# Performance work log

Measured on AMD Instinct MI355X. Metric: run time of the kernel, lower is better.

The kernel has to match this reference:

```python
import jax, jax.numpy as jnp
import numpy as np

B, T, D, H = 4096, 512, 1, 64

def _uniform(k, shape, scale):
    return jax.random.uniform(k, shape, jnp.float32, -scale, scale)

def setup_inputs() -> dict:
    key = jax.random.key(0)
    ks = jax.random.split(key, 12)
    s = 1.0 / np.sqrt(H)  # torch nn.LSTM init scale
    return {
        "x": jax.random.normal(ks[0], (B, T, D), jnp.float32),
        # layer 0 (input_size=D)
        "W_ih0": _uniform(ks[1], (4 * H, D), s),
        "W_hh0": _uniform(ks[2], (4 * H, H), s),
        "b_ih0": _uniform(ks[3], (4 * H,), s),
        "b_hh0": _uniform(ks[4], (4 * H,), s),
        # layer 1 (input_size=H)
        "W_ih1": _uniform(ks[5], (4 * H, H), s),
        "W_hh1": _uniform(ks[6], (4 * H, H), s),
        "b_ih1": _uniform(ks[7], (4 * H,), s),
        "b_hh1": _uniform(ks[8], (4 * H,), s),
        # final projection to scalar
        "W_fc": _uniform(ks[9], (1, H), s),
        "b_fc": _uniform(ks[10], (1,), s),
    }

def _lstm_layer(x_seq, W_ih, W_hh, b_ih, b_hh):
    # x_seq: (B, T, Din) -> hidden sequence (B, T, H). Gate order: i, f, g, o.
    b, t, _ = x_seq.shape
    h = W_hh.shape[1]
    # precompute input contribution for all timesteps: (T, B, 4H)
    x_proj = jnp.einsum('btd,gd->tbg', x_seq, W_ih) + b_ih + b_hh
    Whh_T = W_hh.T  # (H, 4H)

    def step(carry, xp):
        h_t, c_t = carry
        gates = xp + h_t @ Whh_T  # (B, 4H)
        i_g, f_g, g_g, o_g = jnp.split(gates, 4, axis=-1)
        i_g = jax.nn.sigmoid(i_g)
        f_g = jax.nn.sigmoid(f_g)
        g_g = jnp.tanh(g_g)
        o_g = jax.nn.sigmoid(o_g)
        c_t = f_g * c_t + i_g * g_g
        h_t = o_g * jnp.tanh(c_t)
        return (h_t, c_t), h_t

    h0 = jnp.zeros((b, h), x_seq.dtype)
    (_, _), hs = jax.lax.scan(step, (h0, h0), x_proj)  # hs: (T, B, H)
    return jnp.swapaxes(hs, 0, 1)

def reference(x, W_ih0, W_hh0, b_ih0, b_hh0, W_ih1, W_hh1, b_ih1, b_hh1, W_fc, b_fc):
    h1 = _lstm_layer(x, W_ih0, W_hh0, b_ih0, b_hh0)   # (B, T, H)
    h2 = _lstm_layer(h1, W_ih1, W_hh1, b_ih1, b_hh1)  # (B, T, H)
    last = h2[:, -1, :]                                # (B, H)
    return last @ W_fc.T + b_fc                        # (B, 1)
```

## Files before the change

### kernel.cpp

```cpp
#include <hip/hip_runtime.h>


#define TT 512
#define HH 64
#define NB 16
#define XP 516

typedef __bf16 bf16_t;
typedef bf16_t bf16x8 __attribute__((ext_vector_type(8)));
typedef float  f32x4  __attribute__((ext_vector_type(4)));
typedef float  f32x2  __attribute__((ext_vector_type(2)));

#define MFMA(A, B, C) __builtin_amdgcn_mfma_f32_16x16x32_bf16((A), (B), (C), 0, 0, 0)
#define RCPF(x) __builtin_amdgcn_rcpf(x)

#if __has_builtin(__builtin_amdgcn_exp2f)
#define EXP2F(x) __builtin_amdgcn_exp2f(x)
#else
__device__ __forceinline__ float EXP2F(float x) {
    float r;
    asm volatile("v_exp_f32 %0, %1" : "=v"(r) : "v"(x));
    return r;
}
#endif

#define SC_IFO (-1.4426950408889634f)
#define SC_G   ( 2.8853900817779268f)

__device__ __forceinline__ unsigned short f32_to_bf16_rne(float f) {
    unsigned int u = __builtin_bit_cast(unsigned int, f);
    unsigned int r = u + 0x7fffu + ((u >> 16) & 1u);
    return (unsigned short)(r >> 16);
}
__device__ __forceinline__ bf16_t bits_to_bf16(unsigned short u) {
    return __builtin_bit_cast(bf16_t, u);
}
__device__ __forceinline__ void build_frag_scaled(const float* __restrict__ p, float sc,
                                                  bf16x8& w) {
    const float4 a = *(const float4*)p;
    const float4 b = *(const float4*)(p + 4);
    float v[8] = {a.x, a.y, a.z, a.w, b.x, b.y, b.z, b.w};
#pragma unroll
    for (int jj = 0; jj < 8; ++jj)
        w[jj] = bits_to_bf16(f32_to_bf16_rne(v[jj] * sc));
}

__device__ __forceinline__ f32x2 exp2v(f32x2 v) {
    f32x2 r; r[0] = EXP2F(v[0]); r[1] = EXP2F(v[1]); return r;
}
__device__ __forceinline__ f32x2 rcpv(f32x2 v) {
    f32x2 r; r[0] = RCPF(v[0]); r[1] = RCPF(v[1]); return r;
}
__device__ __forceinline__ f32x2 cell2(const f32x4 a0, const f32x4 a1, f32x2* c) {
    f32x2 is = {a0[0], a1[0]}, fs = {a0[1], a1[1]};
    f32x2 gs = {a0[2], a1[2]}, os = {a0[3], a1[3]};
    const f32x2 pf = exp2v(fs);
    const f32x2 fg = rcpv(1.0f + pf);
    const f32x2 pi = exp2v(is);
    const f32x2 e2 = exp2v(gs);
    const f32x2 z  = (e2 - 1.0f) * rcpv((1.0f + pi) * (1.0f + e2));
    *c = fg * (*c) + z;
    const f32x2 po  = exp2v(os);
    const f32x2 e2c = exp2v((*c) * SC_G);
    return (e2c - 1.0f) * rcpv((1.0f + po) * (1.0f + e2c));
}

__device__ __forceinline__ int imin2(int a, int b) { return a < b ? a : b; }
__device__ __forceinline__ int min4of(const int* f) {
    const int4 v = *(const int4*)f;
    return imin2(imin2(v.x, v.y), imin2(v.z, v.w));
}
__device__ __forceinline__ int min8of(const int* f) {
    const int4 a = *(const int4*)f;
    const int4 b = *(const int4*)(f + 4);
    return imin2(imin2(imin2(a.x, a.y), imin2(a.z, a.w)),
                 imin2(imin2(b.x, b.y), imin2(b.z, b.w)));
}

#define SPIN_FUSED(F0, F1, C0, C1)                                              \
    do {                                                                        \
        __builtin_amdgcn_s_setprio(0);                                          \
        for (;;) {                                                              \
            asm volatile("" ::: "memory");                                      \
            if ((min4of(F0) >= (C0)) & (min8of(F1) >= (C1))) break;             \
            asm volatile("" ::: "memory");                                      \
            if ((min4of(F0) >= (C0)) & (min8of(F1) >= (C1))) break;             \
            __builtin_amdgcn_s_sleep(1);                                        \
        }                                                                       \
        __builtin_amdgcn_s_setprio(1);                                          \
    } while (0)

__global__ __launch_bounds__(768, 3)
void lstm_1t_kernel(const float* __restrict__ x,
                    const float* __restrict__ Wih0, const float* __restrict__ Whh0,
                    const float* __restrict__ bih0, const float* __restrict__ bhh0,
                    const float* __restrict__ Wih1, const float* __restrict__ Whh1,
                    const float* __restrict__ bih1, const float* __restrict__ bhh1,
                    const float* __restrict__ Wfc,  const float* __restrict__ bfc,
                    float* __restrict__ out)
{
    __shared__ float xbuf[NB][XP];
    __shared__ unsigned short h0r[8][NB][64];
    __shared__ unsigned short h1r[2][NB][64];
    __shared__ float h1fin[HH][NB + 1];
    __shared__ __align__(16) int f0[4];
    __shared__ __align__(16) int f1[8];

    const int tid  = threadIdx.x;
    const int wv   = tid >> 6;
    const int lane = tid & 63;
    const int m    = lane & 15;
    const int q    = lane >> 4;
    const int m7   = m & 7;
    const int b0   = blockIdx.x * NB;
    const bool isL0 = (wv < 4);

    for (int i = tid; i < NB * TT / 4; i += 768) {
        const int b  = i >> 7;
        const int t4 = i & 127;
        *(float4*)&xbuf[b][t4 * 4] = *(const float4*)&x[(size_t)(b0 + b) * TT + t4 * 4];
    }
    for (int i = tid; i < 8 * NB * 64; i += 768) (&h0r[0][0][0])[i] = 0;
    for (int i = tid; i < 2 * NB * 64; i += 768) (&h1r[0][0][0])[i] = 0;
    if (tid < 4) f0[tid] = -1;
    else if (tid < 12) f1[tid - 4] = -1;

    int roff[2];
#pragma unroll
    for (int kt = 0; kt < 2; ++kt)
        roff[kt] = m * 64 + (((4 * kt + q) ^ m7) * 8);

    const int gate_m = m & 3;
    const float scA  = (gate_m == 2) ? SC_G : SC_IFO;
    unsigned short* const H0 = &h0r[0][0][0];
    unsigned short* const H1 = &h1r[0][0][0];

    __syncthreads();

    __builtin_amdgcn_s_setprio(1);

    if (isL0) {
        const int w = wv;
        bf16x8 Ah[4][2];
        f32x4 bb0s[4], wx0s[4];
        int woff[4];
#pragma unroll
        for (int tau = 0; tau < 4; ++tau) {
            const int rowA = 64 * gate_m + 16 * w + 4 * tau + (m >> 2);
#pragma unroll
            for (int kt = 0; kt < 2; ++kt)
                build_frag_scaled(&Whh0[rowA * HH + kt * 32 + q * 8], scA, Ah[tau][kt]);
#pragma unroll
            for (int r = 0; r < 4; ++r) {
                const int row = 64 * r + 16 * w + 4 * tau + q;
                const float sc = (r == 2) ? SC_G : SC_IFO;
                bb0s[tau][r] = (bih0[row] + bhh0[row]) * sc;
                wx0s[tau][r] = Wih0[row] * sc;
            }
            const int u = 16 * w + 4 * tau + q;
            woff[tau] = m * 64 + (((u >> 3) ^ m7) * 8) + (u & 7);
        }

        f32x2 cA = {0.f, 0.f}, cB = {0.f, 0.f};

#pragma unroll 1
        for (int t = 0; t < TT; ++t) {
            asm volatile("" ::: "memory");
            const int c0 = t - 1;
            const int c1 = t - 8;
            const int rdy = (min4of(f0) >= c0) & (min8of(f1) >= c1);

            const float xv = xbuf[m][t];
            f32x4 a[4];
#pragma unroll
            for (int tau = 0; tau < 4; ++tau) {
#pragma unroll
                for (int r = 0; r < 4; ++r)
                    a[tau][r] = __builtin_fmaf(xv, wx0s[tau][r], bb0s[tau][r]);
            }

            if (!rdy) SPIN_FUSED(f0, f1, c0, c1);
            asm volatile("" ::: "memory");

            const int rs = ((t - 1) & 7) * (NB * 64);
            bf16x8 h0[2];
            h0[0] = *(const bf16x8*)(H0 + rs + roff[0]);
            h0[1] = *(const bf16x8*)(H0 + rs + roff[1]);

#pragma unroll
            for (int tau = 0; tau < 4; ++tau) {
                f32x4 z = {0.f, 0.f, 0.f, 0.f};
                a[tau] = MFMA(Ah[tau][0], h0[0], a[tau]);
                z      = MFMA(Ah[tau][1], h0[1], z);
                a[tau] = a[tau] + z;
            }

            const f32x2 hv0 = cell2(a[0], a[1], &cA);
            const f32x2 hv1 = cell2(a[2], a[3], &cB);

            const int ws = (t & 7) * (NB * 64);
            H0[ws + woff[0]] = f32_to_bf16_rne(hv0[0]);
            H0[ws + woff[1]] = f32_to_bf16_rne(hv0[1]);
            H0[ws + woff[2]] = f32_to_bf16_rne(hv1[0]);
            H0[ws + woff[3]] = f32_to_bf16_rne(hv1[1]);

            asm volatile("s_waitcnt lgkmcnt(0)" ::: "memory");
            if (lane == 0) *(volatile int*)&f0[w] = t;
        }
    } else {
        const int uW = wv - 4;
        bf16x8 Ah[2][4];
        f32x4 bb1s[2];
        int woff[2], uu[2];
#pragma unroll
        for (int tau = 0; tau < 2; ++tau) {
            const int rowA = 64 * gate_m + 8 * uW + 4 * tau + (m >> 2);
#pragma unroll
            for (int kt = 0; kt < 2; ++kt)
                build_frag_scaled(&Wih1[rowA * HH + kt * 32 + q * 8], scA, Ah[tau][kt]);
#pragma unroll
            for (int kt = 0; kt < 2; ++kt)
                build_frag_scaled(&Whh1[rowA * HH + kt * 32 + q * 8], scA, Ah[tau][2 + kt]);
#pragma unroll
            for (int r = 0; r < 4; ++r) {
                const int row = 64 * r + 8 * uW + 4 * tau + q;
                const float sc = (r == 2) ? SC_G : SC_IFO;
                bb1s[tau][r] = (bih1[row] + bhh1[row]) * sc;
            }
            const int u = 8 * uW + 4 * tau + q;
            uu[tau]   = u;
            woff[tau] = m * 64 + (((u >> 3) ^ m7) * 8) + (u & 7);
        }

        f32x2 c1v = {0.f, 0.f};

#pragma unroll 1
        for (int t = 0; t < TT; ++t) {
            asm volatile("" ::: "memory");
            const int c0 = t;
            const int c1 = t - 1;
            if (!((min4of(f0) >= c0) & (min8of(f1) >= c1)))
                SPIN_FUSED(f0, f1, c0, c1);
            asm volatile("" ::: "memory");

            const int rs0 = (t & 7) * (NB * 64);
            const int rs1 = ((t - 1) & 1) * (NB * 64);
            bf16x8 h0[2], h1[2];
            h0[0] = *(const bf16x8*)(H0 + rs0 + roff[0]);
            h0[1] = *(const bf16x8*)(H0 + rs0 + roff[1]);
            h1[0] = *(const bf16x8*)(H1 + rs1 + roff[0]);
            h1[1] = *(const bf16x8*)(H1 + rs1 + roff[1]);

            f32x4 a[2];
#pragma unroll
            for (int tau = 0; tau < 2; ++tau) {
                f32x4 p = bb1s[tau];
                f32x4 s = {0.f, 0.f, 0.f, 0.f};
                p = MFMA(Ah[tau][0], h0[0], p);
                p = MFMA(Ah[tau][1], h0[1], p);
                s = MFMA(Ah[tau][2], h1[0], s);
                s = MFMA(Ah[tau][3], h1[1], s);
                a[tau] = p + s;
            }

            const f32x2 hv = cell2(a[0], a[1], &c1v);
            if (t == TT - 1) {
                h1fin[uu[0]][m] = hv[0];
                h1fin[uu[1]][m] = hv[1];
            }
            const int ws = (t & 1) * (NB * 64);
            H1[ws + woff[0]] = f32_to_bf16_rne(hv[0]);
            H1[ws + woff[1]] = f32_to_bf16_rne(hv[1]);

            asm volatile("s_waitcnt lgkmcnt(0)" ::: "memory");
            if (lane == 0) *(volatile int*)&f1[uW] = t;
        }
    }

    __syncthreads();

    if (tid < NB) {
        float sacc = bfc[0];
#pragma unroll
        for (int u = 0; u < HH; ++u) sacc = fmaf(h1fin[u][tid], Wfc[u], sacc);
        out[b0 + tid] = sacc;
    }
}

extern "C" void kernel_launch(void* const* d_in, const int* in_sizes, int n_in,
                              void* d_out, int out_size, void* d_ws, size_t ws_size,
                              hipStream_t stream) {
    const float* x    = (const float*)d_in[0];
    const float* Wih0 = (const float*)d_in[1];
    const float* Whh0 = (const float*)d_in[2];
    const float* bih0 = (const float*)d_in[3];
    const float* bhh0 = (const float*)d_in[4];
    const float* Wih1 = (const float*)d_in[5];
    const float* Whh1 = (const float*)d_in[6];
    const float* bih1 = (const float*)d_in[7];
    const float* bhh1 = (const float*)d_in[8];
    const float* Wfc  = (const float*)d_in[9];
    const float* bfc  = (const float*)d_in[10];

    lstm_1t_kernel<<<dim3(4096 / NB), dim3(768), 0, stream>>>(
        x, Wih0, Whh0, bih0, bhh0, Wih1, Whh1, bih1, bhh1, Wfc, bfc, (float*)d_out);
}
```

Measured before the change: 492.4 us.

## Split layer-0 across eight waves and split layer-1 waits per input

Raises the block to 1024 threads so layer 0 runs on eight waves with two hidden tiles each instead of four waves with four tiles, shortening each wave's per-step critical path. Layer-1 waves now wait only on the layer-0 flags, issue the input-projection MFMAs, and only then wait on their own recurrent flags before the recurrent MFMAs. This overlaps some of the layer-1 dependency wait with useful work. In exchange there are more waves per block, more flag polling, and possibly fewer resident blocks per CU given the register budget.

```diff
diff --git a/kernel.cpp b/kernel.cpp
--- a/kernel.cpp
+++ b/kernel.cpp
@@ -66,10 +66,6 @@
 }
 
 __device__ __forceinline__ int imin2(int a, int b) { return a < b ? a : b; }
-__device__ __forceinline__ int min4of(const int* f) {
-    const int4 v = *(const int4*)f;
-    return imin2(imin2(v.x, v.y), imin2(v.z, v.w));
-}
 __device__ __forceinline__ int min8of(const int* f) {
     const int4 a = *(const int4*)f;
     const int4 b = *(const int4*)(f + 4);
@@ -77,20 +73,33 @@
                  imin2(imin2(b.x, b.y), imin2(b.z, b.w)));
 }
 
-#define SPIN_FUSED(F0, F1, C0, C1)                                              \
+#define SPIN_BOTH(F0, F1, C0, C1)                                               \
     do {                                                                        \
         __builtin_amdgcn_s_setprio(0);                                          \
         for (;;) {                                                              \
             asm volatile("" ::: "memory");                                      \
-            if ((min4of(F0) >= (C0)) & (min8of(F1) >= (C1))) break;             \
+            if ((min8of(F0) >= (C0)) & (min8of(F1) >= (C1))) break;             \
             asm volatile("" ::: "memory");                                      \
-            if ((min4of(F0) >= (C0)) & (min8of(F1) >= (C1))) break;             \
+            if ((min8of(F0) >= (C0)) & (min8of(F1) >= (C1))) break;             \
             __builtin_amdgcn_s_sleep(1);                                        \
         }                                                                       \
         __builtin_amdgcn_s_setprio(1);                                          \
     } while (0)
 
-__global__ __launch_bounds__(768, 3)
+#define SPIN_ONE(F, C)                                                          \
+    do {                                                                        \
+        __builtin_amdgcn_s_setprio(0);                                          \
+        for (;;) {                                                              \
+            asm volatile("" ::: "memory");                                      \
+            if (min8of(F) >= (C)) break;                                        \
+            asm volatile("" ::: "memory");                                      \
+            if (min8of(F) >= (C)) break;                                        \
+            __builtin_amdgcn_s_sleep(1);                                        \
+        }                                                                       \
+        __builtin_amdgcn_s_setprio(1);                                          \
+    } while (0)
+
+__global__ __launch_bounds__(1024, 4)
 void lstm_1t_kernel(const float* __restrict__ x,
                     const float* __restrict__ Wih0, const float* __restrict__ Whh0,
                     const float* __restrict__ bih0, const float* __restrict__ bhh0,
@@ -103,7 +112,7 @@
     __shared__ unsigned short h0r[8][NB][64];
     __shared__ unsigned short h1r[2][NB][64];
     __shared__ float h1fin[HH][NB + 1];
-    __shared__ __align__(16) int f0[4];
+    __shared__ __align__(16) int f0[8];
     __shared__ __align__(16) int f1[8];
 
     const int tid  = threadIdx.x;
@@ -113,17 +122,17 @@
     const int q    = lane >> 4;
     const int m7   = m & 7;
     const int b0   = blockIdx.x * NB;
-    const bool isL0 = (wv < 4);
-
-    for (int i = tid; i < NB * TT / 4; i += 768) {
+    const bool isL0 = (wv < 8);
+
+    for (int i = tid; i < NB * TT / 4; i += 1024) {
         const int b  = i >> 7;
         const int t4 = i & 127;
         *(float4*)&xbuf[b][t4 * 4] = *(const float4*)&x[(size_t)(b0 + b) * TT + t4 * 4];
     }
-    for (int i = tid; i < 8 * NB * 64; i += 768) (&h0r[0][0][0])[i] = 0;
-    for (int i = tid; i < 2 * NB * 64; i += 768) (&h1r[0][0][0])[i] = 0;
-    if (tid < 4) f0[tid] = -1;
-    else if (tid < 12) f1[tid - 4] = -1;
+    for (int i = tid; i < 8 * NB * 64; i += 1024) (&h0r[0][0][0])[i] = 0;
+    for (int i = tid; i < 2 * NB * 64; i += 1024) (&h1r[0][0][0])[i] = 0;
+    if (tid < 8) f0[tid] = -1;
+    else if (tid < 16) f1[tid - 8] = -1;
 
     int roff[2];
 #pragma unroll
@@ -141,45 +150,45 @@
 
     if (isL0) {
         const int w = wv;
-        bf16x8 Ah[4][2];
-        f32x4 bb0s[4], wx0s[4];
-        int woff[4];
-#pragma unroll
-        for (int tau = 0; tau < 4; ++tau) {
-            const int rowA = 64 * gate_m + 16 * w + 4 * tau + (m >> 2);
+        bf16x8 Ah[2][2];
+        f32x4 bb0s[2], wx0s[2];
+        int woff[2];
+#pragma unroll
+        for (int tau = 0; tau < 2; ++tau) {
+            const int rowA = 64 * gate_m + 8 * w + 4 * tau + (m >> 2);
 #pragma unroll
             for (int kt = 0; kt < 2; ++kt)
                 build_frag_scaled(&Whh0[rowA * HH + kt * 32 + q * 8], scA, Ah[tau][kt]);
 #pragma unroll
             for (int r = 0; r < 4; ++r) {
-                const int row = 64 * r + 16 * w + 4 * tau + q;
+                const int row = 64 * r + 8 * w + 4 * tau + q;
                 const float sc = (r == 2) ? SC_G : SC_IFO;
                 bb0s[tau][r] = (bih0[row] + bhh0[row]) * sc;
                 wx0s[tau][r] = Wih0[row] * sc;
             }
-            const int u = 16 * w + 4 * tau + q;
+            const int u = 8 * w + 4 * tau + q;
             woff[tau] = m * 64 + (((u >> 3) ^ m7) * 8) + (u & 7);
         }
 
-        f32x2 cA = {0.f, 0.f}, cB = {0.f, 0.f};
+        f32x2 cA = {0.f, 0.f};
 
 #pragma unroll 1
         for (int t = 0; t < TT; ++t) {
             asm volatile("" ::: "memory");
             const int c0 = t - 1;
             const int c1 = t - 8;
-            const int rdy = (min4of(f0) >= c0) & (min8of(f1) >= c1);
+            const int rdy = (min8of(f0) >= c0) & (min8of(f1) >= c1);
 
             const float xv = xbuf[m][t];
-            f32x4 a[4];
-#pragma unroll
-            for (int tau = 0; tau < 4; ++tau) {
+            f32x4 a[2];
+#pragma unroll
+            for (int tau = 0; tau < 2; ++tau) {
 #pragma unroll
                 for (int r = 0; r < 4; ++r)
                     a[tau][r] = __builtin_fmaf(xv, wx0s[tau][r], bb0s[tau][r]);
             }
 
-            if (!rdy) SPIN_FUSED(f0, f1, c0, c1);
+            if (!rdy) SPIN_BOTH(f0, f1, c0, c1);
             asm volatile("" ::: "memory");
 
             const int rs = ((t - 1) & 7) * (NB * 64);
@@ -188,27 +197,24 @@
             h0[1] = *(const bf16x8*)(H0 + rs + roff[1]);
 
 #pragma unroll
-            for (int tau = 0; tau < 4; ++tau) {
+            for (int tau = 0; tau < 2; ++tau) {
                 f32x4 z = {0.f, 0.f, 0.f, 0.f};
                 a[tau] = MFMA(Ah[tau][0], h0[0], a[tau]);
                 z      = MFMA(Ah[tau][1], h0[1], z);
                 a[tau] = a[tau] + z;
             }
 
-            const f32x2 hv0 = cell2(a[0], a[1], &cA);
-            const f32x2 hv1 = cell2(a[2], a[3], &cB);
+            const f32x2 hv = cell2(a[0], a[1], &cA);
 
             const int ws = (t & 7) * (NB * 64);
-            H0[ws + woff[0]] = f32_to_bf16_rne(hv0[0]);
-            H0[ws + woff[1]] = f32_to_bf16_rne(hv0[1]);
-            H0[ws + woff[2]] = f32_to_bf16_rne(hv1[0]);
-            H0[ws + woff[3]] = f32_to_bf16_rne(hv1[1]);
+            H0[ws + woff[0]] = f32_to_bf16_rne(hv[0]);
+            H0[ws + woff[1]] = f32_to_bf16_rne(hv[1]);
 
             asm volatile("s_waitcnt lgkmcnt(0)" ::: "memory");
             if (lane == 0) *(volatile int*)&f0[w] = t;
         }
     } else {
-        const int uW = wv - 4;
+        const int uW = wv - 8;
         bf16x8 Ah[2][4];
         f32x4 bb1s[2];
         int woff[2], uu[2];
@@ -237,30 +243,33 @@
 #pragma unroll 1
         for (int t = 0; t < TT; ++t) {
             asm volatile("" ::: "memory");
-            const int c0 = t;
-            const int c1 = t - 1;
-            if (!((min4of(f0) >= c0) & (min8of(f1) >= c1)))
-                SPIN_FUSED(f0, f1, c0, c1);
+            if (min8of(f0) < t) SPIN_ONE(f0, t);
             asm volatile("" ::: "memory");
 
             const int rs0 = (t & 7) * (NB * 64);
-            const int rs1 = ((t - 1) & 1) * (NB * 64);
-            bf16x8 h0[2], h1[2];
+            bf16x8 h0[2];
             h0[0] = *(const bf16x8*)(H0 + rs0 + roff[0]);
             h0[1] = *(const bf16x8*)(H0 + rs0 + roff[1]);
+
+            f32x4 a[2];
+#pragma unroll
+            for (int tau = 0; tau < 2; ++tau) {
+                a[tau] = MFMA(Ah[tau][0], h0[0], bb1s[tau]);
+                a[tau] = MFMA(Ah[tau][1], h0[1], a[tau]);
+            }
+
+            if (min8of(f1) < t - 1) SPIN_ONE(f1, t - 1);
+            asm volatile("" ::: "memory");
+
+            const int rs1 = ((t - 1) & 1) * (NB * 64);
+            bf16x8 h1[2];
             h1[0] = *(const bf16x8*)(H1 + rs1 + roff[0]);
             h1[1] = *(const bf16x8*)(H1 + rs1 + roff[1]);
 
-            f32x4 a[2];
 #pragma unroll
             for (int tau = 0; tau < 2; ++tau) {
-                f32x4 p = bb1s[tau];
-                f32x4 s = {0.f, 0.f, 0.f, 0.f};
-                p = MFMA(Ah[tau][0], h0[0], p);
-                p = MFMA(Ah[tau][1], h0[1], p);
-                s = MFMA(Ah[tau][2], h1[0], s);
-                s = MFMA(Ah[tau][3], h1[1], s);
-                a[tau] = p + s;
+                a[tau] = MFMA(Ah[tau][2], h1[0], a[tau]);
+                a[tau] = MFMA(Ah[tau][3], h1[1], a[tau]);
             }
 
             const f32x2 hv = cell2(a[0], a[1], &c1v);
@@ -302,6 +311,6 @@
     const float* Wfc  = (const float*)d_in[9];
     const float* bfc  = (const float*)d_in[10];
 
-    lstm_1t_kernel<<<dim3(4096 / NB), dim3(768), 0, stream>>>(
+    lstm_1t_kernel<<<dim3(4096 / NB), dim3(1024), 0, stream>>>(
         x, Wih0, Whh0, bih0, bhh0, Wih1, Whh1, bih1, bhh1, Wfc, bfc, (float*)d_out);
 }
```

New measurement: 487.9 us. No clear change (-0.9%).
